# Kernel tuning notes

Hardware: AMD Instinct MI355X
Metric: run time of the kernel (lower is better)

The kernel has to match this reference:

```python
import jax, jax.numpy as jnp
import numpy as np

ALPHA = 0.4  # EMARecurrent(alpha=0.4, learnable=False); forward uses |alpha|


def setup_inputs() -> dict:
    key = jax.random.key(0)
    k1, _ = jax.random.split(key)
    inp = jax.random.normal(k1, (8, 1024, 4096), dtype=jnp.float32)  # [B, D, T]
    hidden = jnp.zeros((8, 1024, 1), dtype=jnp.float32)              # [B, D, 1]
    return {"inp": inp, "hidden": hidden}


def reference(inp, hidden):
    # hidden_t = |a| * x_t + (1 - |a|) * hidden_{t-1}, scanned over axis 2.
    a = jnp.abs(jnp.asarray(ALPHA, dtype=inp.dtype))
    xs = jnp.moveaxis(inp, 2, 0)          # [T, B, D]
    h0 = jnp.squeeze(hidden, axis=2)      # [B, D]

    def step(h, x):
        h = a * x + (1.0 - a) * h
        return h, h

    _, ys = jax.lax.scan(step, h0, xs)    # ys: [T, B, D]
    return jnp.moveaxis(ys, 0, 2)         # [B, D, T]
```

## Files before the change

kernel.cpp:

```cpp
#include <hip/hip_runtime.h>


constexpr int TILES_PER_SEQ = 16;

__global__ __launch_bounds__(256) void ema_tile_kernel(
    const float* __restrict__ x,
    const float* __restrict__ h0,
    float* __restrict__ out,
    int ntiles)
{
    const int gtid = blockIdx.x * blockDim.x + threadIdx.x;
    const int w    = gtid >> 6;
    const int lane = threadIdx.x & 63;
    if (w >= ntiles) return;

    const int tidx = w & (TILES_PER_SEQ - 1);
    const int seq  = w >> 4;

    const float a   = 0.4f;
    const float b   = 0.6f;
    const float b2  = b * b;
    const float b3  = b2 * b;
    const float b4  = b2 * b2;
    const float b8  = b4 * b4;
    const float b16 = b8 * b8;
    const float inv_b4 = 1.0f / b4;

    const float m1 = (lane >= 1) ? b4  : 0.0f;
    const float m2 = (lane >= 2) ? b8  : 0.0f;
    const float m3 = (lane >= 4) ? b16 : 0.0f;
    const float pb4i = exp2f((float)(4 * lane) * -0.73696559416f);

    const float4* __restrict__ xp = (const float4*)x;
    float4* __restrict__ op       = (float4*)out;

    const size_t tile_base = (size_t)w * 64;

    float4 v = xp[tile_base + (size_t)lane];

    const bool has_warm = (tidx != 0);
    float4 wv = make_float4(0.f, 0.f, 0.f, 0.f);
    if (has_warm && lane < 8) {
        wv = xp[tile_base - 8 + (size_t)lane];
    }

    float c0 = a * v.x;
    float c1 = fmaf(b, c0, a * v.y);
    float c2 = fmaf(b, c1, a * v.z);
    float c3 = fmaf(b, c2, a * v.w);

    float t = c3, u;
    u = __shfl_up(t, 1, 64); t = fmaf(m1, u, t);
    u = __shfl_up(t, 2, 64); t = fmaf(m2, u, t);
    u = __shfl_up(t, 4, 64); t = fmaf(m3, u, t);

    float h_in;
    if (has_warm) {
        float d0 = a * wv.x;
        float d1 = fmaf(b, d0, a * wv.y);
        float d2 = fmaf(b, d1, a * wv.z);
        float d3 = fmaf(b, d2, a * wv.w);
        float tw = d3;
        u = __shfl_up(tw, 1, 64); tw = fmaf(m1, u, tw);
        u = __shfl_up(tw, 2, 64); tw = fmaf(m2, u, tw);
        u = __shfl_up(tw, 4, 64); tw = fmaf(m3, u, tw);
        h_in = __shfl(tw, 7, 64);
    } else {
        h_in = h0[(size_t)seq];
    }

    float e = fmaf(pb4i, h_in, (t - c3) * inv_b4);

    float4 o;
    o.x = fmaf(b , e, c0);
    o.y = fmaf(b2, e, c1);
    o.z = fmaf(b3, e, c2);
    o.w = fmaf(b4, e, c3);
    op[tile_base + (size_t)lane] = o;
}

extern "C" void kernel_launch(void* const* d_in, const int* in_sizes, int n_in,
                              void* d_out, int out_size, void* d_ws, size_t ws_size,
                              hipStream_t stream) {
    const float* x  = (const float*)d_in[0];
    const float* h0 = (const float*)d_in[1];
    float* out = (float*)d_out;

    const int nseq   = in_sizes[1];
    const int ntiles = nseq * TILES_PER_SEQ;
    const int block  = 256;
    const long long total = (long long)ntiles * 64;
    const int grid = (int)((total + block - 1) / block);

    ema_tile_kernel<<<grid, block, 0, stream>>>(x, h0, out, ntiles);
}
```

Before: 218.6 us.

## Process two 256-element sub-tiles per wave with exact carry and nontemporal stores

Each wavefront now handles 512 time steps as two 256-element halves. The second half takes its exact incoming state from the last lane of the first half, so only one warm-up window per wave is needed instead of one per 256 elements. The three shuffle-scan chains are interleaved to expose instruction-level parallelism, and the outputs are written with nontemporal stores to avoid polluting the cache. The cost is more registers per thread, half as many waves, and warm-up work that now runs unconditionally.

Result: slower. 228.6 us (+4.6%).

```diff
diff --git a/kernel.cpp b/kernel.cpp
--- a/kernel.cpp
+++ b/kernel.cpp
@@ -1,7 +1,9 @@
 #include <hip/hip_runtime.h>
 
 
-constexpr int TILES_PER_SEQ = 16;
+constexpr int STILES_PER_SEQ = 8;
+
+typedef float fvec4 __attribute__((ext_vector_type(4)));
 
 __global__ __launch_bounds__(256) void ema_tile_kernel(
     const float* __restrict__ x,
@@ -14,8 +16,8 @@
     const int lane = threadIdx.x & 63;
     if (w >= ntiles) return;
 
-    const int tidx = w & (TILES_PER_SEQ - 1);
-    const int seq  = w >> 4;
+    const int sidx = w & (STILES_PER_SEQ - 1);
+    const int seq  = w >> 3;
 
     const float a   = 0.4f;
     const float b   = 0.6f;
@@ -32,51 +34,70 @@
     const float pb4i = exp2f((float)(4 * lane) * -0.73696559416f);
 
     const float4* __restrict__ xp = (const float4*)x;
-    float4* __restrict__ op       = (float4*)out;
+    fvec4* __restrict__ op        = (fvec4*)out;
 
-    const size_t tile_base = (size_t)w * 64;
+    const size_t base = (size_t)w * 128;
 
-    float4 v = xp[tile_base + (size_t)lane];
+    float4 vA = xp[base + (size_t)lane];
+    float4 vB = xp[base + 64 + (size_t)lane];
 
-    const bool has_warm = (tidx != 0);
+    const bool has_warm = (sidx != 0);
     float4 wv = make_float4(0.f, 0.f, 0.f, 0.f);
     if (has_warm && lane < 8) {
-        wv = xp[tile_base - 8 + (size_t)lane];
+        wv = xp[base - 8 + (size_t)lane];
     }
 
-    float c0 = a * v.x;
-    float c1 = fmaf(b, c0, a * v.y);
-    float c2 = fmaf(b, c1, a * v.z);
-    float c3 = fmaf(b, c2, a * v.w);
+    float a0 = a * vA.x;
+    float a1 = fmaf(b, a0, a * vA.y);
+    float a2 = fmaf(b, a1, a * vA.z);
+    float a3 = fmaf(b, a2, a * vA.w);
 
-    float t = c3, u;
-    u = __shfl_up(t, 1, 64); t = fmaf(m1, u, t);
-    u = __shfl_up(t, 2, 64); t = fmaf(m2, u, t);
-    u = __shfl_up(t, 4, 64); t = fmaf(m3, u, t);
+    float c0 = a * vB.x;
+    float c1 = fmaf(b, c0, a * vB.y);
+    float c2 = fmaf(b, c1, a * vB.z);
+    float c3 = fmaf(b, c2, a * vB.w);
+
+    float d0 = a * wv.x;
+    float d1 = fmaf(b, d0, a * wv.y);
+    float d2 = fmaf(b, d1, a * wv.z);
+    float d3 = fmaf(b, d2, a * wv.w);
+
+    float tA = a3, tB = c3, tw = d3, u;
+    u = __shfl_up(tA, 1, 64); tA = fmaf(m1, u, tA);
+    u = __shfl_up(tB, 1, 64); tB = fmaf(m1, u, tB);
+    u = __shfl_up(tw, 1, 64); tw = fmaf(m1, u, tw);
+    u = __shfl_up(tA, 2, 64); tA = fmaf(m2, u, tA);
+    u = __shfl_up(tB, 2, 64); tB = fmaf(m2, u, tB);
+    u = __shfl_up(tw, 2, 64); tw = fmaf(m2, u, tw);
+    u = __shfl_up(tA, 4, 64); tA = fmaf(m3, u, tA);
+    u = __shfl_up(tB, 4, 64); tB = fmaf(m3, u, tB);
+    u = __shfl_up(tw, 4, 64); tw = fmaf(m3, u, tw);
 
     float h_in;
     if (has_warm) {
-        float d0 = a * wv.x;
-        float d1 = fmaf(b, d0, a * wv.y);
-        float d2 = fmaf(b, d1, a * wv.z);
-        float d3 = fmaf(b, d2, a * wv.w);
-        float tw = d3;
-        u = __shfl_up(tw, 1, 64); tw = fmaf(m1, u, tw);
-        u = __shfl_up(tw, 2, 64); tw = fmaf(m2, u, tw);
-        u = __shfl_up(tw, 4, 64); tw = fmaf(m3, u, tw);
         h_in = __shfl(tw, 7, 64);
     } else {
         h_in = h0[(size_t)seq];
     }
 
-    float e = fmaf(pb4i, h_in, (t - c3) * inv_b4);
+    float eA = fmaf(pb4i, h_in, (tA - a3) * inv_b4);
+    fvec4 oA;
+    oA.x = fmaf(b , eA, a0);
+    oA.y = fmaf(b2, eA, a1);
+    oA.z = fmaf(b3, eA, a2);
+    oA.w = fmaf(b4, eA, a3);
 
-    float4 o;
-    o.x = fmaf(b , e, c0);
-    o.y = fmaf(b2, e, c1);
-    o.z = fmaf(b3, e, c2);
-    o.w = fmaf(b4, e, c3);
-    op[tile_base + (size_t)lane] = o;
+    float h_mid = __shfl(oA.w, 63, 64);
+
+    float eB = fmaf(pb4i, h_mid, (tB - c3) * inv_b4);
+    fvec4 oB;
+    oB.x = fmaf(b , eB, c0);
+    oB.y = fmaf(b2, eB, c1);
+    oB.z = fmaf(b3, eB, c2);
+    oB.w = fmaf(b4, eB, c3);
+
+    __builtin_nontemporal_store(oA, &op[base + (size_t)lane]);
+    __builtin_nontemporal_store(oB, &op[base + 64 + (size_t)lane]);
 }
 
 extern "C" void kernel_launch(void* const* d_in, const int* in_sizes, int n_in,
@@ -87,7 +108,7 @@
     float* out = (float*)d_out;
 
     const int nseq   = in_sizes[1];
-    const int ntiles = nseq * TILES_PER_SEQ;
+    const int ntiles = nseq * STILES_PER_SEQ;
     const int block  = 256;
     const long long total = (long long)ntiles * 64;
     const int grid = (int)((total + block - 1) / block);
```
